# Kernel tuning notes

Hardware: AMD Instinct MI355X
Metric: run time of the kernel (lower is better)

The kernel has to match this reference:

```python
import jax, jax.numpy as jnp
import numpy as np

FEA, ATT, HLAST, STEP = 256, 64, 10, 12
H = FEA * HLAST  # lstm hidden/cell size = 2560
IN = 2 * H       # concat(input, hidden) = 5120


def setup_inputs() -> dict:
    key = jax.random.key(0)
    ks = jax.random.split(key, 16)
    s = lambda k, shp, fan: jax.random.normal(k, shp, jnp.float32) * (1.0 / np.sqrt(fan))
    return {
        "x": jax.random.normal(ks[0], (64 * STEP, FEA, ATT), jnp.float32),
        # encoder: Linear(64->128), Linear(128->10) (stored as [in,out])
        "W0": s(ks[1], (ATT, 128), ATT), "b0": jnp.zeros((128,), jnp.float32),
        "W1": s(ks[2], (128, HLAST), 128), "b1": jnp.zeros((HLAST,), jnp.float32),
        # LSTM gates: forget, input, output, cell  [IN, H]
        "Wf": s(ks[3], (IN, H), IN), "bf": jnp.zeros((H,), jnp.float32),
        "Wi": s(ks[4], (IN, H), IN), "bi": jnp.zeros((H,), jnp.float32),
        "Wo": s(ks[5], (IN, H), IN), "bo": jnp.zeros((H,), jnp.float32),
        "Wc": s(ks[6], (IN, H), IN), "bc": jnp.zeros((H,), jnp.float32),
        # final fc: Linear(10->10)
        "Wfc": s(ks[7], (HLAST, HLAST), HLAST), "bfc": jnp.zeros((HLAST,), jnp.float32),
    }


def reference(x, W0, b0, W1, b1, Wf, bf, Wi, bi, Wo, bo, Wc, bc, Wfc, bfc):
    # encoder (dropout is identity at eval): Linear -> ReLU, twice
    h = x.reshape(-1, FEA, ATT)
    h = jax.nn.relu(h @ W0 + b0)            # [B*T, FEA, 128]
    h = jax.nn.relu(h @ W1 + b1)            # [B*T, FEA, 10]
    h = h.reshape(-1, STEP, H)              # [B, T, H]
    B = h.shape[0]

    def step_fn(carry, xt):
        hs, cs = carry                       # [B, H] each
        comb = jnp.concatenate([xt, hs], axis=1)  # [B, 2H]
        f = jax.nn.sigmoid(comb @ Wf + bf)
        i = jax.nn.sigmoid(comb @ Wi + bi)
        o = jax.nn.sigmoid(comb @ Wo + bo)
        g = jnp.tanh(comb @ Wc + bc)
        cs = f * cs + i * g
        hs = o * jnp.tanh(cs)
        return (hs, cs), None

    init = (jnp.zeros((B, H), h.dtype), jnp.zeros((B, H), h.dtype))
    (hs, _), _ = jax.lax.scan(step_fn, init, jnp.swapaxes(h, 0, 1))  # scan over time

    out = hs.reshape(B, FEA, HLAST)          # [B, 256, 10]
    out = jax.nn.relu(out) @ Wfc + bfc       # fc(ReLU(x))
    return out
```

## Files before the change

### kernel.cpp

```cpp
#include <hip/hip_runtime.h>
#include <math.h>

#define FEA   256
#define ATT   64
#define HLAST 10
#define NSTEP 12
#define HDIM  2560
#define BATCH 64
#define BT    768
#define KT_FULL 160
#define KT_HALF 80
#define NT_G  160
#define MT_E  48

typedef _Float16 h8_t __attribute__((ext_vector_type(8)));
typedef float    f4_t __attribute__((ext_vector_type(4)));

__device__ __forceinline__ float sigm(float x) { return 1.0f / (1.0f + expf(-x)); }

__global__ __launch_bounds__(256) void k_convert_w(
    const float* __restrict__ Wf, const float* __restrict__ Wi,
    const float* __restrict__ Wo, const float* __restrict__ Wc,
    _Float16* __restrict__ Wp)
{
  __shared__ float tile[32][130];
  const int bid = blockIdx.x;
  const int g = bid / (KT_FULL * 20);
  const int r = bid % (KT_FULL * 20);
  const int kt = r / 20, cb = r % 20;
  const float* __restrict__ W = (g == 0) ? Wf : (g == 1) ? Wi : (g == 2) ? Wo : Wc;
  const float* src = W + (size_t)(kt * 32) * HDIM + cb * 128;
  const int tid = threadIdx.x;
  #pragma unroll
  for (int s = 0; s < 4; ++s) {
    const int slot = s * 256 + tid;
    const int rr = slot >> 5, c4 = slot & 31;
    float4 v = *(const float4*)&src[(size_t)rr * HDIM + c4 * 4];
    *(float4*)&tile[rr][c4 * 4] = v;
  }
  __syncthreads();
  const int l = tid & 63, w = tid >> 6;
  const int k0 = (l >> 4) * 8, c16 = l & 15;
  #pragma unroll
  for (int s = 0; s < 2; ++s) {
    const int f = w * 2 + s;
    h8_t h;
    #pragma unroll
    for (int j = 0; j < 8; ++j) h[j] = (_Float16)tile[k0 + j][f * 16 + c16];
    const int nt = cb * 8 + f;
    *(h8_t*)&Wp[(((size_t)(g * NT_G + nt) * KT_FULL + kt) << 9) + l * 8] = h;
  }
}

__global__ __launch_bounds__(256) void k_pack_enc(
    const float* __restrict__ W0, const float* __restrict__ W1,
    _Float16* __restrict__ Bp0, _Float16* __restrict__ Bp1)
{
  const int tid = threadIdx.x;
  for (int e = tid; e < 16 * 512; e += 256) {
    const int frag = e >> 9, idx = e & 511, l = idx >> 3, j = idx & 7;
    const int nt = frag >> 1, kt = frag & 1;
    const int k = kt * 32 + (l >> 4) * 8 + j;
    const int n = nt * 16 + (l & 15);
    Bp0[e] = (_Float16)W0[k * 128 + n];
  }
  for (int e = tid; e < 4 * 512; e += 256) {
    const int kt = e >> 9, idx = e & 511, l = idx >> 3, j = idx & 7;
    const int k = kt * 32 + (l >> 4) * 8 + j;
    const int n = l & 15;
    Bp1[e] = (n < HLAST) ? (_Float16)W1[k * HLAST + n] : (_Float16)0.0f;
  }
}

__global__ __launch_bounds__(256) void k_enc2(
    const float* __restrict__ x, const _Float16* __restrict__ Bp0,
    const _Float16* __restrict__ Bp1, const float* __restrict__ b0,
    const float* __restrict__ b1, _Float16* __restrict__ Ep)
{
  __shared__ __align__(16) _Float16 sA[4][16][136];
  const int tid = threadIdx.x, l = tid & 63, w = tid >> 6;
  const int bt = blockIdx.x >> 2;
  const int f0 = (blockIdx.x & 3) * 64 + w * 16;
  const int rl = l >> 4, cl = l & 15;

  h8_t B0[16];
  #pragma unroll
  for (int q = 0; q < 16; ++q)
    B0[q] = *(const h8_t*)(Bp0 + (q << 9) + l * 8);

  const float* xr = x + ((size_t)bt * FEA + f0 + cl) * ATT + rl * 8;
  h8_t a0, a1;
  {
    float4 v0 = *(const float4*)(xr);
    float4 v1 = *(const float4*)(xr + 4);
    float4 v2 = *(const float4*)(xr + 32);
    float4 v3 = *(const float4*)(xr + 36);
    #pragma unroll
    for (int j = 0; j < 4; ++j) {
      a0[j]     = (_Float16)((const float*)&v0)[j];
      a0[4 + j] = (_Float16)((const float*)&v1)[j];
      a1[j]     = (_Float16)((const float*)&v2)[j];
      a1[4 + j] = (_Float16)((const float*)&v3)[j];
    }
  }
  f4_t acc1[8] = {};
  #pragma unroll
  for (int j = 0; j < 8; ++j) {
    acc1[j] = __builtin_amdgcn_mfma_f32_16x16x32_f16(a0, B0[j * 2 + 0], acc1[j], 0, 0, 0);
    acc1[j] = __builtin_amdgcn_mfma_f32_16x16x32_f16(a1, B0[j * 2 + 1], acc1[j], 0, 0, 0);
  }
  #pragma unroll
  for (int j = 0; j < 8; ++j) {
    const float bj = b0[j * 16 + cl];
    #pragma unroll
    for (int r = 0; r < 4; ++r)
      sA[w][rl * 4 + r][j * 16 + cl] = (_Float16)fmaxf(acc1[j][r] + bj, 0.0f);
  }
  f4_t acc2 = {};
  #pragma unroll
  for (int kt = 0; kt < 4; ++kt) {
    const h8_t a = *(const h8_t*)&sA[w][cl][kt * 32 + rl * 8];
    const h8_t b = *(const h8_t*)(Bp1 + (kt << 9) + l * 8);
    acc2 = __builtin_amdgcn_mfma_f32_16x16x32_f16(a, b, acc2, 0, 0, 0);
  }
  if (cl < HLAST) {
    const float b1v = b1[cl];
    #pragma unroll
    for (int r = 0; r < 4; ++r) {
      const int f = f0 + rl * 4 + r;
      const float val = fmaxf(acc2[r] + b1v, 0.0f);
      const int kf = f * HLAST + cl;
      const int mt = bt >> 4, kt2 = kf >> 5, gp = (kf >> 3) & 3, jj = kf & 7;
      Ep[(((size_t)mt * KT_HALF + kt2) << 9) + (((bt & 15) + 16 * gp) << 3) + jj] =
          (_Float16)val;
    }
  }
}

__global__ __launch_bounds__(512) void k_xpre(
    const _Float16* __restrict__ Ep, const _Float16* __restrict__ Wp,
    const float* __restrict__ bf, const float* __restrict__ bi,
    const float* __restrict__ bo, const float* __restrict__ bc,
    _Float16* __restrict__ Xpre)
{
  __shared__ __align__(16) _Float16 sB[2][32 * 512];
  const int g = blockIdx.z, mh = blockIdx.y;
  const float* __restrict__ bias = (g == 0) ? bf : (g == 1) ? bi : (g == 2) ? bo : bc;
  const int nt0 = blockIdx.x * 4;
  const int tid = threadIdx.x, l = tid & 63, w = tid >> 6;
  const int mt0 = mh * 24 + w * 3;
  const _Float16* Bsrc = Wp + ((size_t)(g * NT_G + nt0) * KT_FULL) * 512 + l * 8;
  const _Float16* Asrc = Ep + ((size_t)mt0 * KT_HALF) * 512 + l * 8;

  f4_t acc[3][4] = {};

#define STAGE_XPRE(cc, buf)                                                       \
  {                                                                               \
    _Pragma("unroll")                                                             \
    for (int s = 0; s < 4; ++s) {                                                 \
      const int fi = s * 8 + w;                                                   \
      const int jj = fi >> 3, tt = fi & 7;                                        \
      const _Float16* gsrc = Bsrc + ((size_t)jj * KT_FULL + (cc) * 8 + tt) * 512; \
      __builtin_amdgcn_global_load_lds(                                           \
          (const __attribute__((address_space(1))) unsigned int*)(const void*)gsrc, \
          (__attribute__((address_space(3))) unsigned int*)(void*)&sB[buf][fi * 512], \
          16, 0, 0);                                                              \
    }                                                                             \
  }

  STAGE_XPRE(0, 0);
  __syncthreads();
  for (int cc = 0; cc < 10; ++cc) {
    const int buf = cc & 1;
    if (cc < 9) STAGE_XPRE(cc + 1, buf ^ 1);
    #pragma unroll
    for (int t = 0; t < 8; ++t) {
      const int kt = cc * 8 + t;
      h8_t b[4], a[3];
      #pragma unroll
      for (int j = 0; j < 4; ++j)
        b[j] = *(const h8_t*)&sB[buf][(j * 8 + t) * 512 + l * 8];
      #pragma unroll
      for (int i = 0; i < 3; ++i)
        a[i] = *(const h8_t*)(Asrc + ((size_t)i * KT_HALF + kt) * 512);
      #pragma unroll
      for (int i = 0; i < 3; ++i)
        #pragma unroll
        for (int j = 0; j < 4; ++j)
          acc[i][j] = __builtin_amdgcn_mfma_f32_16x16x32_f16(a[i], b[j], acc[i][j], 0, 0, 0);
    }
    __syncthreads();
  }

  const int rl = l >> 4, cl = l & 15;
  const int bn = nt0 * 16;
  #pragma unroll
  for (int j = 0; j < 4; ++j) {
    const int n = bn + j * 16 + cl;
    const float bv = bias[n];
    #pragma unroll
    for (int i = 0; i < 3; ++i)
      #pragma unroll
      for (int r = 0; r < 4; ++r) {
        const int m = (mt0 + i) * 16 + rl * 4 + r;
        Xpre[((size_t)g * BT + m) * HDIM + n] = (_Float16)(acc[i][j][r] + bv);
      }
  }
#undef STAGE_XPRE
}

__global__ __launch_bounds__(512) void k_step(
    const _Float16* __restrict__ hP, const _Float16* __restrict__ Wp,
    const _Float16* __restrict__ Xpre, float* __restrict__ cbuf,
    float* __restrict__ hbuf, _Float16* __restrict__ hPn, int tstep)
{
  __shared__ float pre_lds[8][32 * 17];
  const int tid = threadIdx.x, l = tid & 63, w = tid >> 6;
  const int g = w >> 1, kc = w & 1;
  const int nt = blockIdx.x, mh = blockIdx.y;
  const int kt0 = kc * 40;
  const int dir = tstep & 1;
  const int base = dir ? (kt0 + 39) : kt0;
  const int sgn = dir ? -1 : 1;

  const int ub = tid >> 4, un = tid & 15;
  const int brow = mh * 32 + ub;
  const int unf = nt * 16 + un;
  const size_t xr = ((size_t)brow * NSTEP + tstep) * HDIM + unf;
  const float xf = (float)Xpre[xr];
  const float xi = (float)Xpre[(size_t)1 * BT * HDIM + xr];
  const float xo = (float)Xpre[(size_t)2 * BT * HDIM + xr];
  const float xc = (float)Xpre[(size_t)3 * BT * HDIM + xr];
  const size_t ci = (size_t)brow * HDIM + unf;
  const float cold = cbuf[ci];

  const _Float16* Ab = hP + (((size_t)mh * 2 * KT_HALF) << 9) + l * 8;
  const _Float16* Bb = Wp + (((size_t)(g * NT_G + nt) * KT_FULL + KT_HALF) << 9) + l * 8;

  f4_t acc[2] = {};
  h8_t bq[12];
  #pragma unroll
  for (int s = 0; s < 12; ++s)
    bq[s] = *(const h8_t*)(Bb + ((size_t)(base + sgn * s) << 9));
  h8_t aq[4][2];
  #pragma unroll
  for (int s = 0; s < 4; ++s)
    #pragma unroll
    for (int i = 0; i < 2; ++i)
      aq[s][i] = *(const h8_t*)(Ab + (((size_t)(i * KT_HALF + base + sgn * s)) << 9));

  #pragma unroll
  for (int it = 0; it < 40; ++it) {
    const int kt = base + sgn * it;
    const h8_t bcur = bq[it % 12];
    const h8_t a0 = aq[it & 3][0], a1 = aq[it & 3][1];
    if (it < 28)
      bq[it % 12] = *(const h8_t*)(Bb + ((size_t)(kt + sgn * 12) << 9));
    if (it < 36) {
      aq[it & 3][0] = *(const h8_t*)(Ab + (((size_t)(0 * KT_HALF + kt + sgn * 4)) << 9));
      aq[it & 3][1] = *(const h8_t*)(Ab + (((size_t)(1 * KT_HALF + kt + sgn * 4)) << 9));
    }
    acc[0] = __builtin_amdgcn_mfma_f32_16x16x32_f16(a0, bcur, acc[0], 0, 0, 0);
    acc[1] = __builtin_amdgcn_mfma_f32_16x16x32_f16(a1, bcur, acc[1], 0, 0, 0);
  }

  float* pl = pre_lds[w];
  const int rl = l >> 4, cl = l & 15;
  #pragma unroll
  for (int i = 0; i < 2; ++i)
    #pragma unroll
    for (int r = 0; r < 4; ++r)
      pl[(i * 16 + rl * 4 + r) * 17 + cl] = acc[i][r];
  __syncthreads();
  {
    const int off = ub * 17 + un;
    float pf = xf, pi_ = xi, po = xo, pc = xc;
    #pragma unroll
    for (int kc2 = 0; kc2 < 2; ++kc2) {
      pf  += pre_lds[0 * 2 + kc2][off];
      pi_ += pre_lds[1 * 2 + kc2][off];
      po  += pre_lds[2 * 2 + kc2][off];
      pc  += pre_lds[3 * 2 + kc2][off];
    }
    const float f = sigm(pf), i_ = sigm(pi_), o = sigm(po), gg = tanhf(pc);
    const float cn = f * cold + i_ * gg;
    cbuf[ci] = cn;
    const float hn = o * tanhf(cn);
    if (tstep == NSTEP - 1) hbuf[ci] = hn;
    const int mt = brow >> 4, kt2 = unf >> 5, gp = (unf >> 3) & 3, j = unf & 7;
    hPn[(((size_t)mt * KT_HALF + kt2) << 9) + ((brow & 15) + 16 * gp) * 8 + j] = (_Float16)hn;
  }
}

__global__ __launch_bounds__(256) void k_out(
    const float* __restrict__ h, const float* __restrict__ Wfc,
    const float* __restrict__ bfc, float* __restrict__ out)
{
  __shared__ float sW[HLAST * HLAST], sb[HLAST];
  const int t = threadIdx.x;
  if (t < HLAST * HLAST) sW[t] = Wfc[t];
  if (t < HLAST) sb[t] = bfc[t];
  __syncthreads();
  const int idx = blockIdx.x * 256 + t;
  const int j = idx % HLAST;
  const int bf_ = idx / HLAST;
  float a = sb[j];
  #pragma unroll
  for (int k = 0; k < HLAST; ++k)
    a = fmaf(fmaxf(h[(size_t)bf_ * HLAST + k], 0.0f), sW[k * HLAST + j], a);
  out[idx] = a;
}

extern "C" void kernel_launch(void* const* d_in, const int* in_sizes, int n_in,
                              void* d_out, int out_size, void* d_ws, size_t ws_size,
                              hipStream_t stream)
{
  const float* x   = (const float*)d_in[0];
  const float* W0  = (const float*)d_in[1];
  const float* b0  = (const float*)d_in[2];
  const float* W1  = (const float*)d_in[3];
  const float* b1  = (const float*)d_in[4];
  const float* Wf  = (const float*)d_in[5];
  const float* bfp = (const float*)d_in[6];
  const float* Wi  = (const float*)d_in[7];
  const float* bip = (const float*)d_in[8];
  const float* Wo  = (const float*)d_in[9];
  const float* bop = (const float*)d_in[10];
  const float* Wc  = (const float*)d_in[11];
  const float* bcp = (const float*)d_in[12];
  const float* Wfc = (const float*)d_in[13];
  const float* bfc = (const float*)d_in[14];

  char* ws = (char*)d_ws;
  _Float16* Wp = (_Float16*)ws;                       ws += (size_t)4 * NT_G * KT_FULL * 512 * 2;
  _Float16* Ep = (_Float16*)ws;                       ws += (size_t)MT_E * KT_HALF * 512 * 2;
  _Float16* Xpre = (_Float16*)ws;                     ws += (size_t)4 * BT * HDIM * 2;
  float* cbuf  = (float*)ws;                          ws += (size_t)BATCH * HDIM * 4;
  float* hbuf  = (float*)ws;                          ws += (size_t)BATCH * HDIM * 4;
  _Float16* hPa = (_Float16*)ws;                      ws += (size_t)BATCH * HDIM * 2;
  _Float16* hPb = (_Float16*)ws;                      ws += (size_t)BATCH * HDIM * 2;
  _Float16* Bp0 = (_Float16*)ws;                      ws += (size_t)16 * 512 * 2;
  _Float16* Bp1 = (_Float16*)ws;                      ws += (size_t)4 * 512 * 2;

  hipMemsetAsync(cbuf, 0, (size_t)BATCH * HDIM * 4, stream);
  hipMemsetAsync(hPa, 0, (size_t)BATCH * HDIM * 2, stream);

  k_pack_enc<<<1, 256, 0, stream>>>(W0, W1, Bp0, Bp1);
  k_enc2<<<BT * 4, 256, 0, stream>>>(x, Bp0, Bp1, b0, b1, Ep);
  k_convert_w<<<4 * KT_FULL * 20, 256, 0, stream>>>(Wf, Wi, Wo, Wc, Wp);
  k_xpre<<<dim3(HDIM / 64, 2, 4), 512, 0, stream>>>(
      Ep, Wp, bfp, bip, bop, bcp, Xpre);
  _Float16* hin = hPa;
  _Float16* hout = hPb;
  for (int t = 0; t < NSTEP; ++t) {
    k_step<<<dim3(NT_G, 2), 512, 0, stream>>>(hin, Wp, Xpre, cbuf, hbuf, hout, t);
    _Float16* tmp = hin; hin = hout; hout = tmp;
  }
  k_out<<<(BATCH * FEA * HLAST) / 256, 256, 0, stream>>>(hbuf, Wfc, bfc, (float*)d_out);
}
```

Measured before the change: 378.1 us.

## Overlap weight fp16 conversion with encoder and input-projection kernels

Removes the standalone weight-conversion kernel and spreads its blocks across the encoder and xpre launches. The first half of the K tiles (input part) is converted alongside the encoder; the second half (hidden part, only needed by the recurrent steps) is converted inside the xpre launch, interleaved with the GEMM blocks. This overlaps memory-bound conversion with compute and saves a launch. The cost is more complex block indexing, and the xpre GEMM blocks now share the GPU with conversion blocks.

```diff
diff --git a/kernel.cpp b/kernel.cpp
--- a/kernel.cpp
+++ b/kernel.cpp
@@ -18,40 +18,6 @@
 
 __device__ __forceinline__ float sigm(float x) { return 1.0f / (1.0f + expf(-x)); }
 
-__global__ __launch_bounds__(256) void k_convert_w(
-    const float* __restrict__ Wf, const float* __restrict__ Wi,
-    const float* __restrict__ Wo, const float* __restrict__ Wc,
-    _Float16* __restrict__ Wp)
-{
-  __shared__ float tile[32][130];
-  const int bid = blockIdx.x;
-  const int g = bid / (KT_FULL * 20);
-  const int r = bid % (KT_FULL * 20);
-  const int kt = r / 20, cb = r % 20;
-  const float* __restrict__ W = (g == 0) ? Wf : (g == 1) ? Wi : (g == 2) ? Wo : Wc;
-  const float* src = W + (size_t)(kt * 32) * HDIM + cb * 128;
-  const int tid = threadIdx.x;
-  #pragma unroll
-  for (int s = 0; s < 4; ++s) {
-    const int slot = s * 256 + tid;
-    const int rr = slot >> 5, c4 = slot & 31;
-    float4 v = *(const float4*)&src[(size_t)rr * HDIM + c4 * 4];
-    *(float4*)&tile[rr][c4 * 4] = v;
-  }
-  __syncthreads();
-  const int l = tid & 63, w = tid >> 6;
-  const int k0 = (l >> 4) * 8, c16 = l & 15;
-  #pragma unroll
-  for (int s = 0; s < 2; ++s) {
-    const int f = w * 2 + s;
-    h8_t h;
-    #pragma unroll
-    for (int j = 0; j < 8; ++j) h[j] = (_Float16)tile[k0 + j][f * 16 + c16];
-    const int nt = cb * 8 + f;
-    *(h8_t*)&Wp[(((size_t)(g * NT_G + nt) * KT_FULL + kt) << 9) + l * 8] = h;
-  }
-}
-
 __global__ __launch_bounds__(256) void k_pack_enc(
     const float* __restrict__ W0, const float* __restrict__ W1,
     _Float16* __restrict__ Bp0, _Float16* __restrict__ Bp1)
@@ -72,15 +38,52 @@
   }
 }
 
-__global__ __launch_bounds__(256) void k_enc2(
+__global__ __launch_bounds__(256) void k_enc_conv(
     const float* __restrict__ x, const _Float16* __restrict__ Bp0,
     const _Float16* __restrict__ Bp1, const float* __restrict__ b0,
-    const float* __restrict__ b1, _Float16* __restrict__ Ep)
+    const float* __restrict__ b1, _Float16* __restrict__ Ep,
+    const float* __restrict__ Wf, const float* __restrict__ Wi,
+    const float* __restrict__ Wo, const float* __restrict__ Wc,
+    _Float16* __restrict__ Wp)
 {
   __shared__ __align__(16) _Float16 sA[4][16][136];
-  const int tid = threadIdx.x, l = tid & 63, w = tid >> 6;
-  const int bt = blockIdx.x >> 2;
-  const int f0 = (blockIdx.x & 3) * 64 + w * 16;
+  const int grp = blockIdx.x / 37, r37 = blockIdx.x % 37;
+  const int tid = threadIdx.x;
+
+  if (r37 >= 12) {
+    float (*tile)[130] = (float(*)[130])(void*)sA;
+    const int cid = grp * 25 + (r37 - 12);
+    const int g = cid / 1600;
+    const int r = cid % 1600;
+    const int kt = r / 20, cb = r % 20;
+    const float* __restrict__ W = (g == 0) ? Wf : (g == 1) ? Wi : (g == 2) ? Wo : Wc;
+    const float* src = W + (size_t)(kt * 32) * HDIM + cb * 128;
+    #pragma unroll
+    for (int s = 0; s < 4; ++s) {
+      const int slot = s * 256 + tid;
+      const int rr = slot >> 5, c4 = slot & 31;
+      float4 v = *(const float4*)&src[(size_t)rr * HDIM + c4 * 4];
+      *(float4*)&tile[rr][c4 * 4] = v;
+    }
+    __syncthreads();
+    const int l = tid & 63, w = tid >> 6;
+    const int k0 = (l >> 4) * 8, c16 = l & 15;
+    #pragma unroll
+    for (int s = 0; s < 2; ++s) {
+      const int f = w * 2 + s;
+      h8_t h;
+      #pragma unroll
+      for (int j = 0; j < 8; ++j) h[j] = (_Float16)tile[k0 + j][f * 16 + c16];
+      const int nt = cb * 8 + f;
+      *(h8_t*)&Wp[(((size_t)(g * NT_G + nt) * KT_FULL + kt) << 9) + l * 8] = h;
+    }
+    return;
+  }
+
+  const int eid = grp * 12 + r37;
+  const int l = tid & 63, w = tid >> 6;
+  const int bt = eid >> 2;
+  const int f0 = (eid & 3) * 64 + w * 16;
   const int rl = l >> 4, cl = l & 15;
 
   h8_t B0[16];
@@ -137,17 +140,49 @@
   }
 }
 
-__global__ __launch_bounds__(512) void k_xpre(
-    const _Float16* __restrict__ Ep, const _Float16* __restrict__ Wp,
+__global__ __launch_bounds__(512) void k_xpre_conv(
+    const _Float16* __restrict__ Ep, _Float16* __restrict__ Wp,
     const float* __restrict__ bf, const float* __restrict__ bi,
     const float* __restrict__ bo, const float* __restrict__ bc,
-    _Float16* __restrict__ Xpre)
+    _Float16* __restrict__ Xpre,
+    const float* __restrict__ Wf, const float* __restrict__ Wi,
+    const float* __restrict__ Wo, const float* __restrict__ Wc)
 {
   __shared__ __align__(16) _Float16 sB[2][32 * 512];
-  const int g = blockIdx.z, mh = blockIdx.y;
+  const int bid = blockIdx.x, tid = threadIdx.x;
+
+  if (bid % 21 != 0) {
+    float (*tile)[130] = (float(*)[130])(void*)sB;
+    const int cid = bid - bid / 21 - 1;
+    const int g = cid / 1600;
+    const int r = cid % 1600;
+    const int kt = 80 + r / 20, cb = r % 20;
+    const float* __restrict__ W = (g == 0) ? Wf : (g == 1) ? Wi : (g == 2) ? Wo : Wc;
+    const float* src = W + (size_t)(kt * 32) * HDIM + cb * 128;
+    #pragma unroll
+    for (int s = 0; s < 2; ++s) {
+      const int slot = s * 512 + tid;
+      const int rr = slot >> 5, c4 = slot & 31;
+      float4 v = *(const float4*)&src[(size_t)rr * HDIM + c4 * 4];
+      *(float4*)&tile[rr][c4 * 4] = v;
+    }
+    __syncthreads();
+    const int l = tid & 63, f = tid >> 6;
+    const int k0 = (l >> 4) * 8, c16 = l & 15;
+    h8_t h;
+    #pragma unroll
+    for (int j = 0; j < 8; ++j) h[j] = (_Float16)tile[k0 + j][f * 16 + c16];
+    const int nt = cb * 8 + f;
+    *(h8_t*)&Wp[(((size_t)(g * NT_G + nt) * KT_FULL + kt) << 9) + l * 8] = h;
+    return;
+  }
+
+  const int rid = bid / 21;
+  const int bx = rid % 40, by = (rid / 40) & 1, bz = rid / 80;
+  const int g = bz, mh = by;
   const float* __restrict__ bias = (g == 0) ? bf : (g == 1) ? bi : (g == 2) ? bo : bc;
-  const int nt0 = blockIdx.x * 4;
-  const int tid = threadIdx.x, l = tid & 63, w = tid >> 6;
+  const int nt0 = bx * 4;
+  const int l = tid & 63, w = tid >> 6;
   const int mt0 = mh * 24 + w * 3;
   const _Float16* Bsrc = Wp + ((size_t)(g * NT_G + nt0) * KT_FULL) * 512 + l * 8;
   const _Float16* Asrc = Ep + ((size_t)mt0 * KT_HALF) * 512 + l * 8;
@@ -346,10 +381,10 @@
   hipMemsetAsync(hPa, 0, (size_t)BATCH * HDIM * 2, stream);
 
   k_pack_enc<<<1, 256, 0, stream>>>(W0, W1, Bp0, Bp1);
-  k_enc2<<<BT * 4, 256, 0, stream>>>(x, Bp0, Bp1, b0, b1, Ep);
-  k_convert_w<<<4 * KT_FULL * 20, 256, 0, stream>>>(Wf, Wi, Wo, Wc, Wp);
-  k_xpre<<<dim3(HDIM / 64, 2, 4), 512, 0, stream>>>(
-      Ep, Wp, bfp, bip, bop, bcp, Xpre);
+  k_enc_conv<<<37 * 256, 256, 0, stream>>>(x, Bp0, Bp1, b0, b1, Ep,
+                                           Wf, Wi, Wo, Wc, Wp);
+  k_xpre_conv<<<21 * 320, 512, 0, stream>>>(Ep, Wp, bfp, bip, bop, bcp, Xpre,
+                                            Wf, Wi, Wo, Wc);
   _Float16* hin = hPa;
   _Float16* hout = hPb;
   for (int t = 0; t < NSTEP; ++t) {
```

New measurement: 378.9 us. About the same (+0.2%).
